# Performance work log

Measured on AMD Instinct MI355X. Metric: run time of the kernel, lower is better.

The kernel has to match this reference:

```python
import jax, jax.numpy as jnp
import numpy as np

B, S, D, H = 2, 2048, 1024, 16
HD = D // H  # head_dim = 64


def setup_inputs() -> dict:
    key = jax.random.key(0)
    ks = jax.random.split(key, 12)
    s = 1.0 / np.sqrt(D)
    return {
        "query": jax.random.normal(ks[0], (B, S, D), jnp.float32),
        "key": jax.random.normal(ks[1], (B, S, D), jnp.float32),
        "value": jax.random.normal(ks[2], (B, S, D), jnp.float32),
        "attention_mask": jnp.zeros((B, S, S), jnp.float32),
        "WQ_w": jax.random.normal(ks[3], (D, D), jnp.float32) * s,
        "WQ_b": jnp.zeros((D,), jnp.float32),
        "WK_w": jax.random.normal(ks[4], (D, D), jnp.float32) * s,
        "WK_b": jnp.zeros((D,), jnp.float32),
        "WV_w": jax.random.normal(ks[5], (D, D), jnp.float32) * s,
        "WV_b": jnp.zeros((D,), jnp.float32),
        "WO_w": jax.random.normal(ks[6], (D, D), jnp.float32) * s,
        "WO_b": jnp.zeros((D,), jnp.float32),
    }


def _split_heads(x):
    # [B,S,D] -> [B,H,S,HD]
    b, s, _ = x.shape
    return x.reshape(b, s, H, HD).transpose(0, 2, 1, 3)


def reference(query, key, value, attention_mask,
              WQ_w, WQ_b, WK_w, WK_b, WV_w, WV_b, WO_w, WO_b):
    Q = _split_heads(query @ WQ_w.T + WQ_b)   # [B,H,S,HD]
    K = _split_heads(key @ WK_w.T + WK_b)
    V = _split_heads(value @ WV_w.T + WV_b)
    scale = 1.0 / jnp.sqrt(jnp.float32(HD))
    scores = jnp.einsum('bhqd,bhkd->bhqk', Q, K) * scale
    scores = scores + attention_mask[:, None, :, :]
    attn = jax.nn.softmax(scores, axis=-1)    # dropout_prob=0.0 -> identity
    out = jnp.einsum('bhqk,bhkd->bhqd', attn, V)
    out = out.transpose(0, 2, 1, 3).reshape(query.shape[0], -1, D)
    return out @ WO_w.T + WO_b
```

## Files before the change

### kernel.cpp

```cpp
#include <hip/hip_runtime.h>
#include <math.h>


typedef _Float16 h8 __attribute__((ext_vector_type(8)));
typedef _Float16 h4 __attribute__((ext_vector_type(4)));
typedef float f4 __attribute__((ext_vector_type(4)));

#define MFMA16(a, b, c) __builtin_amdgcn_mfma_f32_16x16x32_f16((a), (b), (c), 0, 0, 0)
#define EXP2F(x) __builtin_amdgcn_exp2f(x)

static constexpr int Bn = 2, Sn = 2048, Dn = 1024, Hn = 16, HDn = 64;
static constexpr int Mn = Bn * Sn;
static constexpr int Kn = Dn;
static constexpr int Nn = Dn;
static constexpr int LDP = 72;
static constexpr float LOG2E = 1.4426950408889634f;

__device__ __forceinline__ void gload_lds16(const _Float16* g, _Float16* l) {
  __builtin_amdgcn_global_load_lds(
      (const __attribute__((address_space(1))) unsigned int*)g,
      (__attribute__((address_space(3))) unsigned int*)l, 16, 0, 0);
}

struct CvtJobs {
  const float* src[8];
  _Float16* dst[8];
  int n4[8];
  float scl[8];
};

__global__ __launch_bounds__(256) void cvt_kernel(CvtJobs j) {
  const int stride = gridDim.x * blockDim.x;
  const int t0 = blockIdx.x * blockDim.x + threadIdx.x;
#pragma unroll
  for (int k = 0; k < 8; ++k) {
    const float4* __restrict__ s = (const float4*)j.src[k];
    h4* __restrict__ d = (h4*)j.dst[k];
    const int n = j.n4[k];
    const float sc = j.scl[k];
    for (int i = t0; i < n; i += stride) {
      const float4 f = s[i];
      h4 h;
      h[0] = (_Float16)(f.x * sc); h[1] = (_Float16)(f.y * sc);
      h[2] = (_Float16)(f.z * sc); h[3] = (_Float16)(f.w * sc);
      d[i] = h;
    }
  }
}

struct QkvArgs {
  const _Float16* X[3];
  const _Float16* W[3];
  const float* bias[3];
  _Float16* out[3];
};

__global__ __launch_bounds__(256) void gemm_qkv(QkvArgs args) {
  const int z = blockIdx.z;
  const _Float16* __restrict__ X = args.X[z];
  const _Float16* __restrict__ W = args.W[z];
  const float* __restrict__ bias = args.bias[z];
  _Float16* __restrict__ out = args.out[z];

  __shared__ _Float16 As[128 * 64];
  __shared__ _Float16 Bs[128 * 64];

  const int t = threadIdx.x;
  const int lane = t & 63, wv = t >> 6;
  const int l15 = lane & 15, quad = lane >> 4;
  const int wm = (wv >> 1) * 64, wn = (wv & 1) * 64;
  const int n0 = blockIdx.x * 128, m0 = blockIdx.y * 128;

  f4 acc[4][4];
#pragma unroll
  for (int i = 0; i < 4; ++i)
#pragma unroll
    for (int j = 0; j < 4; ++j) {
      f4 zz = {0.f, 0.f, 0.f, 0.f};
      acc[i][j] = zz;
    }

  const int srow = lane >> 3, scol = (lane & 7) * 8;

  for (int k0 = 0; k0 < Kn; k0 += 64) {
    __syncthreads();
#pragma unroll
    for (int u = 0; u < 4; ++u) {
      const int s = wv * 4 + u;
      const int row = s * 8 + srow;
      gload_lds16(X + (size_t)(m0 + row) * Kn + k0 + scol, As + s * 512);
      gload_lds16(W + (size_t)(n0 + row) * Kn + k0 + scol, Bs + s * 512);
    }
    __syncthreads();
#pragma unroll
    for (int kk = 0; kk < 64; kk += 32) {
      h8 af[4], bfr[4];
#pragma unroll
      for (int i = 0; i < 4; ++i)
        af[i] = *(const h8*)&As[(wm + i * 16 + l15) * 64 + kk + quad * 8];
#pragma unroll
      for (int j = 0; j < 4; ++j)
        bfr[j] = *(const h8*)&Bs[(wn + j * 16 + l15) * 64 + kk + quad * 8];
#pragma unroll
      for (int i = 0; i < 4; ++i)
#pragma unroll
        for (int j = 0; j < 4; ++j)
          acc[i][j] = MFMA16(af[i], bfr[j], acc[i][j]);
    }
  }

  const float osc = (z == 0) ? (0.125f * LOG2E) : 1.0f;
  if (z != 2) {
#pragma unroll
    for (int j = 0; j < 4; ++j) {
      const int n = n0 + wn + j * 16 + l15;
      const float bvs = bias[n] * osc;
      const int hh = n >> 6, hd = n & 63;
#pragma unroll
      for (int i = 0; i < 4; ++i) {
        const int mb = m0 + wm + i * 16 + quad * 4;
        const int bb = mb >> 11;
#pragma unroll
        for (int r = 0; r < 4; ++r) {
          const int ss = (mb + r) & (Sn - 1);
          out[(((size_t)(bb * Hn + hh)) * Sn + ss) * HDn + hd] =
              (_Float16)(acc[i][j][r] * osc + bvs);
        }
      }
    }
  } else {
#pragma unroll
    for (int j = 0; j < 4; ++j) {
      const int n = n0 + wn + j * 16 + l15;
      const float bv = bias[n];
      const int hh = n >> 6, hd = n & 63;
#pragma unroll
      for (int i = 0; i < 4; ++i) {
        const int mb = m0 + wm + i * 16 + quad * 4;
        const int bb = mb >> 11, ss = mb & (Sn - 1);
        h4 hv;
#pragma unroll
        for (int r = 0; r < 4; ++r) hv[r] = (_Float16)(acc[i][j][r] + bv);
        *(h4*)(out + (((size_t)(bb * Hn + hh)) * HDn + hd) * Sn + ss) = hv;
      }
    }
  }
}

__global__ __launch_bounds__(256) void gemm_o(const _Float16* __restrict__ X,
                                              const _Float16* __restrict__ W,
                                              const float* __restrict__ bias,
                                              float* __restrict__ out) {
  __shared__ _Float16 As[128 * 64];
  __shared__ _Float16 Bs[128 * 64];

  const int t = threadIdx.x;
  const int lane = t & 63, wv = t >> 6;
  const int l15 = lane & 15, quad = lane >> 4;
  const int wm = (wv >> 1) * 64, wn = (wv & 1) * 64;
  const int n0 = blockIdx.x * 128, m0 = blockIdx.y * 128;

  f4 acc[4][4];
#pragma unroll
  for (int i = 0; i < 4; ++i)
#pragma unroll
    for (int j = 0; j < 4; ++j) {
      f4 zz = {0.f, 0.f, 0.f, 0.f};
      acc[i][j] = zz;
    }

  const int srow = lane >> 3, scol = (lane & 7) * 8;

  for (int k0 = 0; k0 < Kn; k0 += 64) {
    __syncthreads();
#pragma unroll
    for (int u = 0; u < 4; ++u) {
      const int s = wv * 4 + u;
      const int row = s * 8 + srow;
      gload_lds16(X + (size_t)(m0 + row) * Kn + k0 + scol, As + s * 512);
      gload_lds16(W + (size_t)(n0 + row) * Kn + k0 + scol, Bs + s * 512);
    }
    __syncthreads();
#pragma unroll
    for (int kk = 0; kk < 64; kk += 32) {
      h8 af[4], bfr[4];
#pragma unroll
      for (int i = 0; i < 4; ++i)
        af[i] = *(const h8*)&As[(wm + i * 16 + l15) * 64 + kk + quad * 8];
#pragma unroll
      for (int j = 0; j < 4; ++j)
        bfr[j] = *(const h8*)&Bs[(wn + j * 16 + l15) * 64 + kk + quad * 8];
#pragma unroll
      for (int i = 0; i < 4; ++i)
#pragma unroll
        for (int j = 0; j < 4; ++j)
          acc[i][j] = MFMA16(af[i], bfr[j], acc[i][j]);
    }
  }

#pragma unroll
  for (int j = 0; j < 4; ++j) {
    const int n = n0 + wn + j * 16 + l15;
    const float bv = bias[n];
#pragma unroll
    for (int i = 0; i < 4; ++i) {
      const int mb = m0 + wm + i * 16 + quad * 4;
#pragma unroll
      for (int r = 0; r < 4; ++r)
        out[(size_t)(mb + r) * Nn + n] = acc[i][j][r] + bv;
    }
  }
}

__global__ __launch_bounds__(512) void attn_kernel(
    const _Float16* __restrict__ Qh,
    const _Float16* __restrict__ Kh,
    const _Float16* __restrict__ Vt,
    const _Float16* __restrict__ maskh,
    _Float16* __restrict__ out) {
  __shared__ _Float16 smem[4 * 64 * LDP];

  const int t = threadIdx.x;
  const int w = t >> 6, lane = t & 63;
  const int l15 = lane & 15, quad = lane >> 4;
  const int g = w >> 2;
  const int wq = w & 3;

  const int bid = blockIdx.y * gridDim.x + blockIdx.x;
  const int xcd = bid & 7;
  const int idx = bid >> 3;
  const int bh = (xcd << 2) | (idx >> 5);
  const int qb = (idx & 31) * 64;

  const int b = bh >> 4, h = bh & 15;
  const size_t headoff = (size_t)bh * Sn * HDn;
  const _Float16* Qp = Qh + headoff;
  const _Float16* Kp = Kh + headoff;
  const _Float16* Vp = Vt + headoff;

  const int q0 = qb + wq * 16;
  const h8 qf0 = *(const h8*)(Qp + (size_t)(q0 + l15) * HDn + quad * 8);
  const h8 qf1 = *(const h8*)(Qp + (size_t)(q0 + l15) * HDn + 32 + quad * 8);

  const int kbase = g * (Sn / 2);
  const _Float16* mrow = maskh + ((size_t)b * Sn + q0 + l15) * Sn + kbase;

  float m_run = -INFINITY, l_part = 0.f;
  f4 o_acc[4];
#pragma unroll
  for (int nt = 0; nt < 4; ++nt) {
    f4 zz = {0.f, 0.f, 0.f, 0.f};
    o_acc[nt] = zz;
  }

  _Float16* Kg = smem + g * (64 * LDP);
  _Float16* Vg = smem + (2 + g) * (64 * LDP);

  const int tg = t & 255;
  const int srow = tg >> 3, sc8 = (tg & 7) * 8;
  const int srow1 = srow + 32;
  const int a = tg & 7;
  const int vb = ((a >> 2) & 1) * 32 + (a & 1) * 16 + ((a >> 1) & 1) * 4;

  constexpr int NT = (Sn / 2) / 64;

  uint4 kreg0, kreg1, vreg0, vreg1;
  uint2 mreg[4];
  auto kv_issue = [&](int kt) {
    kreg0 = *(const uint4*)(Kp + (size_t)(kbase + kt * 64 + srow) * HDn + sc8);
    vreg0 = *(const uint4*)(Vp + (size_t)srow * Sn + kbase + kt * 64 + sc8);
    kreg1 = *(const uint4*)(Kp + (size_t)(kbase + kt * 64 + srow1) * HDn + sc8);
    vreg1 = *(const uint4*)(Vp + (size_t)srow1 * Sn + kbase + kt * 64 + sc8);
  };
  auto m_issue = [&](int kt) {
#pragma unroll
    for (int ks = 0; ks < 4; ++ks)
      mreg[ks] = *(const uint2*)(mrow + kt * 64 + ks * 16 + quad * 4);
  };

  kv_issue(0);
  m_issue(0);

  for (int kt = 0; kt < NT; ++kt) {
    __syncthreads();
    *(uint4*)&Kg[srow * LDP + sc8] = kreg0;
    *(uint4*)&Kg[srow1 * LDP + sc8] = kreg1;
    *(uint2*)&Vg[srow * LDP + vb] = make_uint2(vreg0.x, vreg0.y);
    *(uint2*)&Vg[srow * LDP + vb + 8] = make_uint2(vreg0.z, vreg0.w);
    *(uint2*)&Vg[srow1 * LDP + vb] = make_uint2(vreg1.x, vreg1.y);
    *(uint2*)&Vg[srow1 * LDP + vb + 8] = make_uint2(vreg1.z, vreg1.w);
    __syncthreads();
    const int nx = (kt + 1 < NT) ? kt + 1 : kt;
    kv_issue(nx);

    f4 s[4];
#pragma unroll
    for (int ks = 0; ks < 4; ++ks) {
      const h4 mh = *(const h4*)&mreg[ks];
      f4 acc0;
#pragma unroll
      for (int r = 0; r < 4; ++r) acc0[r] = (float)mh[r];
      const h8 kf0 = *(const h8*)&Kg[(ks * 16 + l15) * LDP + quad * 8];
      const h8 kf1 = *(const h8*)&Kg[(ks * 16 + l15) * LDP + 32 + quad * 8];
      acc0 = MFMA16(kf0, qf0, acc0);
      s[ks] = MFMA16(kf1, qf1, acc0);
    }
    m_issue(nx);

    float mx = s[0][0];
#pragma unroll
    for (int ks = 0; ks < 4; ++ks)
#pragma unroll
      for (int r = 0; r < 4; ++r) mx = fmaxf(mx, s[ks][r]);
    mx = fmaxf(mx, __shfl_xor(mx, 16));
    mx = fmaxf(mx, __shfl_xor(mx, 32));
    if (!__all(mx - m_run <= 8.0f)) {
      const float nm = fmaxf(m_run, mx);
      const float alpha = EXP2F(m_run - nm);
      m_run = nm;
      l_part *= alpha;
#pragma unroll
      for (int nt = 0; nt < 4; ++nt)
#pragma unroll
        for (int r = 0; r < 4; ++r) o_acc[nt][r] *= alpha;
    }
    float sm = 0.f;
#pragma unroll
    for (int ks = 0; ks < 4; ++ks)
#pragma unroll
      for (int r = 0; r < 4; ++r) {
        s[ks][r] = EXP2F(s[ks][r] - m_run);
        sm += s[ks][r];
      }
    l_part += sm;

#pragma unroll
    for (int c = 0; c < 2; ++c) {
      h8 pf;
#pragma unroll
      for (int r = 0; r < 4; ++r) pf[r] = (_Float16)s[2 * c][r];
#pragma unroll
      for (int r = 0; r < 4; ++r) pf[4 + r] = (_Float16)s[2 * c + 1][r];
#pragma unroll
      for (int nt = 0; nt < 4; ++nt) {
        const h8 vf = *(const h8*)&Vg[(nt * 16 + l15) * LDP + c * 32 + quad * 8];
        o_acc[nt] = MFMA16(vf, pf, o_acc[nt]);
      }
    }
  }

  l_part += __shfl_xor(l_part, 16);
  l_part += __shfl_xor(l_part, 32);

  __syncthreads();
  float* Uex = (float*)smem;
  float* mex = Uex + 4 * 16 * LDP;
  float* lex = mex + 64;
  if (g == 1) {
#pragma unroll
    for (int nt = 0; nt < 4; ++nt)
      *(f4*)&Uex[wq * 16 * LDP + l15 * LDP + nt * 16 + quad * 4] = o_acc[nt];
    if (quad == 0) {
      mex[wq * 16 + l15] = m_run;
      lex[wq * 16 + l15] = l_part;
    }
  }
  __syncthreads();
  if (g == 0) {
    const float m1 = mex[wq * 16 + l15];
    const float l1 = lex[wq * 16 + l15];
    const float mm = fmaxf(m_run, m1);
    const float f0 = EXP2F(m_run - mm);
    const float f1 = EXP2F(m1 - mm);
    const float rl = 1.0f / (f0 * l_part + f1 * l1);
    _Float16* Ob = smem + 3 * (64 * LDP) + (w * 16) * LDP;
#pragma unroll
    for (int nt = 0; nt < 4; ++nt) {
      const f4 Ur = *(const f4*)&Uex[wq * 16 * LDP + l15 * LDP + nt * 16 + quad * 4];
      h4 ov;
#pragma unroll
      for (int r = 0; r < 4; ++r)
        ov[r] = (_Float16)((o_acc[nt][r] * f0 + Ur[r] * f1) * rl);
      *(h4*)&Ob[l15 * LDP + nt * 16 + quad * 4] = ov;
    }
    const int qr = lane >> 2;
    const int seg = (lane & 3) * 16;
    _Float16* dst = out + ((size_t)b * Sn + q0 + qr) * Dn + h * 64 + seg;
    *(uint4*)dst = *(const uint4*)&Ob[qr * LDP + seg];
    *(uint4*)(dst + 8) = *(const uint4*)&Ob[qr * LDP + seg + 8];
  }
}

extern "C" void kernel_launch(void* const* d_in, const int* in_sizes, int n_in,
                              void* d_out, int out_size, void* d_ws, size_t ws_size,
                              hipStream_t stream) {
  const float* q = (const float*)d_in[0];
  const float* k = (const float*)d_in[1];
  const float* v = (const float*)d_in[2];
  const float* mask = (const float*)d_in[3];
  const float* WQ = (const float*)d_in[4];
  const float* bQ = (const float*)d_in[5];
  const float* WK = (const float*)d_in[6];
  const float* bK = (const float*)d_in[7];
  const float* WV = (const float*)d_in[8];
  const float* bV = (const float*)d_in[9];
  const float* WO = (const float*)d_in[10];
  const float* bO = (const float*)d_in[11];

  _Float16* ws = (_Float16*)d_ws;
  const size_t MD = (size_t)Mn * Dn;
  const size_t DD = (size_t)Dn * Dn;
  const size_t SS = (size_t)Bn * Sn * Sn;
  _Float16* qh  = ws;
  _Float16* kh  = ws + MD;
  _Float16* vh  = ws + 2 * MD;
  _Float16* WQh = ws + 3 * MD;
  _Float16* WKh = WQh + DD;
  _Float16* WVh = WKh + DD;
  _Float16* WOh = WVh + DD;
  _Float16* Qh  = ws + 3 * MD + 4 * DD;
  _Float16* Kh  = Qh + MD;
  _Float16* Vt  = Kh + MD;
  _Float16* AO  = qh;
  const size_t used = 6 * MD + 4 * DD;
  _Float16* Mh = (ws_size >= (used + SS) * sizeof(_Float16))
                     ? (ws + used)
                     : (_Float16*)d_out;

  CvtJobs cj;
  cj.src[0] = q;    cj.dst[0] = qh;  cj.n4[0] = (int)(MD / 4);  cj.scl[0] = 1.f;
  cj.src[1] = k;    cj.dst[1] = kh;  cj.n4[1] = (int)(MD / 4);  cj.scl[1] = 1.f;
  cj.src[2] = v;    cj.dst[2] = vh;  cj.n4[2] = (int)(MD / 4);  cj.scl[2] = 1.f;
  cj.src[3] = WQ;   cj.dst[3] = WQh; cj.n4[3] = (int)(DD / 4);  cj.scl[3] = 1.f;
  cj.src[4] = WK;   cj.dst[4] = WKh; cj.n4[4] = (int)(DD / 4);  cj.scl[4] = 1.f;
  cj.src[5] = WV;   cj.dst[5] = WVh; cj.n4[5] = (int)(DD / 4);  cj.scl[5] = 1.f;
  cj.src[6] = WO;   cj.dst[6] = WOh; cj.n4[6] = (int)(DD / 4);  cj.scl[6] = 1.f;
  cj.src[7] = mask; cj.dst[7] = Mh;  cj.n4[7] = (int)(SS / 4);  cj.scl[7] = LOG2E;
  cvt_kernel<<<1024, 256, 0, stream>>>(cj);

  QkvArgs ga;
  ga.X[0] = qh; ga.W[0] = WQh; ga.bias[0] = bQ; ga.out[0] = Qh;
  ga.X[1] = kh; ga.W[1] = WKh; ga.bias[1] = bK; ga.out[1] = Kh;
  ga.X[2] = vh; ga.W[2] = WVh; ga.bias[2] = bV; ga.out[2] = Vt;
  gemm_qkv<<<dim3(Nn / 128, Mn / 128, 3), 256, 0, stream>>>(ga);

  attn_kernel<<<dim3(Sn / 64, Bn * Hn), 512, 0, stream>>>(Qh, Kh, Vt, Mh, AO);

  gemm_o<<<dim3(Nn / 128, Mn / 128), 256, 0, stream>>>(AO, WOh, bO, (float*)d_out);
}
```

Measured before the change: 305.0 us.

## Process two query sub-tiles per wave in attention to reuse K/V tiles

Each attention block now handles 128 query rows instead of 64, with every wave computing two 16-row query sub-tiles that share the same K and V fragments read from LDS. This halves global K/V traffic and LDS staging per query and raises MFMA work per load. It also drops the XCD-aware block remapping and adds a launch-bounds occupancy hint. The costs are higher register pressure, half as many blocks (512), and a two-pass epilogue with extra barriers.

```diff
diff --git a/kernel.cpp b/kernel.cpp
--- a/kernel.cpp
+++ b/kernel.cpp
@@ -212,7 +212,7 @@
   }
 }
 
-__global__ __launch_bounds__(512) void attn_kernel(
+__global__ __launch_bounds__(512, 4) void attn_kernel(
     const _Float16* __restrict__ Qh,
     const _Float16* __restrict__ Kh,
     const _Float16* __restrict__ Vt,
@@ -226,31 +226,32 @@
   const int g = w >> 2;
   const int wq = w & 3;
 
-  const int bid = blockIdx.y * gridDim.x + blockIdx.x;
-  const int xcd = bid & 7;
-  const int idx = bid >> 3;
-  const int bh = (xcd << 2) | (idx >> 5);
-  const int qb = (idx & 31) * 64;
-
+  const int bh = blockIdx.y;
   const int b = bh >> 4, h = bh & 15;
   const size_t headoff = (size_t)bh * Sn * HDn;
   const _Float16* Qp = Qh + headoff;
   const _Float16* Kp = Kh + headoff;
   const _Float16* Vp = Vt + headoff;
 
-  const int q0 = qb + wq * 16;
-  const h8 qf0 = *(const h8*)(Qp + (size_t)(q0 + l15) * HDn + quad * 8);
-  const h8 qf1 = *(const h8*)(Qp + (size_t)(q0 + l15) * HDn + 32 + quad * 8);
+  const int qb = blockIdx.x * 128;
+  const int q0 = qb + wq * 32;
+  const h8 qf00 = *(const h8*)(Qp + (size_t)(q0 + l15) * HDn + quad * 8);
+  const h8 qf01 = *(const h8*)(Qp + (size_t)(q0 + l15) * HDn + 32 + quad * 8);
+  const h8 qf10 = *(const h8*)(Qp + (size_t)(q0 + 16 + l15) * HDn + quad * 8);
+  const h8 qf11 = *(const h8*)(Qp + (size_t)(q0 + 16 + l15) * HDn + 32 + quad * 8);
 
   const int kbase = g * (Sn / 2);
-  const _Float16* mrow = maskh + ((size_t)b * Sn + q0 + l15) * Sn + kbase;
-
-  float m_run = -INFINITY, l_part = 0.f;
-  f4 o_acc[4];
+  const _Float16* mrow0 = maskh + ((size_t)b * Sn + q0 + l15) * Sn + kbase;
+  const _Float16* mrow1 = mrow0 + (size_t)16 * Sn;
+
+  float m_run0 = -INFINITY, l_part0 = 0.f;
+  float m_run1 = -INFINITY, l_part1 = 0.f;
+  f4 o0[4], o1[4];
 #pragma unroll
   for (int nt = 0; nt < 4; ++nt) {
     f4 zz = {0.f, 0.f, 0.f, 0.f};
-    o_acc[nt] = zz;
+    o0[nt] = zz;
+    o1[nt] = zz;
   }
 
   _Float16* Kg = smem + g * (64 * LDP);
@@ -265,7 +266,7 @@
   constexpr int NT = (Sn / 2) / 64;
 
   uint4 kreg0, kreg1, vreg0, vreg1;
-  uint2 mreg[4];
+  uint2 mreg0[4], mreg1[4];
   auto kv_issue = [&](int kt) {
     kreg0 = *(const uint4*)(Kp + (size_t)(kbase + kt * 64 + srow) * HDn + sc8);
     vreg0 = *(const uint4*)(Vp + (size_t)srow * Sn + kbase + kt * 64 + sc8);
@@ -274,8 +275,10 @@
   };
   auto m_issue = [&](int kt) {
 #pragma unroll
-    for (int ks = 0; ks < 4; ++ks)
-      mreg[ks] = *(const uint2*)(mrow + kt * 64 + ks * 16 + quad * 4);
+    for (int ks = 0; ks < 4; ++ks) {
+      mreg0[ks] = *(const uint2*)(mrow0 + kt * 64 + ks * 16 + quad * 4);
+      mreg1[ks] = *(const uint2*)(mrow1 + kt * 64 + ks * 16 + quad * 4);
+    }
   };
 
   kv_issue(0);
@@ -293,101 +296,154 @@
     const int nx = (kt + 1 < NT) ? kt + 1 : kt;
     kv_issue(nx);
 
-    f4 s[4];
+    f4 s0[4], s1[4];
 #pragma unroll
     for (int ks = 0; ks < 4; ++ks) {
-      const h4 mh = *(const h4*)&mreg[ks];
-      f4 acc0;
-#pragma unroll
-      for (int r = 0; r < 4; ++r) acc0[r] = (float)mh[r];
       const h8 kf0 = *(const h8*)&Kg[(ks * 16 + l15) * LDP + quad * 8];
       const h8 kf1 = *(const h8*)&Kg[(ks * 16 + l15) * LDP + 32 + quad * 8];
-      acc0 = MFMA16(kf0, qf0, acc0);
-      s[ks] = MFMA16(kf1, qf1, acc0);
+      const h4 mh0 = *(const h4*)&mreg0[ks];
+      const h4 mh1 = *(const h4*)&mreg1[ks];
+      f4 a0, a1;
+#pragma unroll
+      for (int r = 0; r < 4; ++r) { a0[r] = (float)mh0[r]; a1[r] = (float)mh1[r]; }
+      a0 = MFMA16(kf0, qf00, a0);
+      s0[ks] = MFMA16(kf1, qf01, a0);
+      a1 = MFMA16(kf0, qf10, a1);
+      s1[ks] = MFMA16(kf1, qf11, a1);
     }
     m_issue(nx);
 
-    float mx = s[0][0];
-#pragma unroll
-    for (int ks = 0; ks < 4; ++ks)
-#pragma unroll
-      for (int r = 0; r < 4; ++r) mx = fmaxf(mx, s[ks][r]);
-    mx = fmaxf(mx, __shfl_xor(mx, 16));
-    mx = fmaxf(mx, __shfl_xor(mx, 32));
-    if (!__all(mx - m_run <= 8.0f)) {
-      const float nm = fmaxf(m_run, mx);
-      const float alpha = EXP2F(m_run - nm);
-      m_run = nm;
-      l_part *= alpha;
-#pragma unroll
-      for (int nt = 0; nt < 4; ++nt)
-#pragma unroll
-        for (int r = 0; r < 4; ++r) o_acc[nt][r] *= alpha;
-    }
-    float sm = 0.f;
-#pragma unroll
-    for (int ks = 0; ks < 4; ++ks)
-#pragma unroll
-      for (int r = 0; r < 4; ++r) {
-        s[ks][r] = EXP2F(s[ks][r] - m_run);
-        sm += s[ks][r];
-      }
-    l_part += sm;
+    h8 pf0[2], pf1[2];
+    {
+      float mx = s0[0][0];
+#pragma unroll
+      for (int ks = 0; ks < 4; ++ks)
+#pragma unroll
+        for (int r = 0; r < 4; ++r) mx = fmaxf(mx, s0[ks][r]);
+      mx = fmaxf(mx, __shfl_xor(mx, 16));
+      mx = fmaxf(mx, __shfl_xor(mx, 32));
+      if (!__all(mx - m_run0 <= 8.0f)) {
+        const float nm = fmaxf(m_run0, mx);
+        const float al = EXP2F(m_run0 - nm);
+        m_run0 = nm;
+        l_part0 *= al;
+#pragma unroll
+        for (int nt = 0; nt < 4; ++nt)
+#pragma unroll
+          for (int r = 0; r < 4; ++r) o0[nt][r] *= al;
+      }
+      float sm = 0.f;
+#pragma unroll
+      for (int ks = 0; ks < 4; ++ks)
+#pragma unroll
+        for (int r = 0; r < 4; ++r) {
+          s0[ks][r] = EXP2F(s0[ks][r] - m_run0);
+          sm += s0[ks][r];
+        }
+      l_part0 += sm;
+#pragma unroll
+      for (int c = 0; c < 2; ++c)
+#pragma unroll
+        for (int r = 0; r < 4; ++r) {
+          pf0[c][r] = (_Float16)s0[2 * c][r];
+          pf0[c][4 + r] = (_Float16)s0[2 * c + 1][r];
+        }
+    }
+    {
+      float mx = s1[0][0];
+#pragma unroll
+      for (int ks = 0; ks < 4; ++ks)
+#pragma unroll
+        for (int r = 0; r < 4; ++r) mx = fmaxf(mx, s1[ks][r]);
+      mx = fmaxf(mx, __shfl_xor(mx, 16));
+      mx = fmaxf(mx, __shfl_xor(mx, 32));
+      if (!__all(mx - m_run1 <= 8.0f)) {
+        const float nm = fmaxf(m_run1, mx);
+        const float al = EXP2F(m_run1 - nm);
+        m_run1 = nm;
+        l_part1 *= al;
+#pragma unroll
+        for (int nt = 0; nt < 4; ++nt)
+#pragma unroll
+          for (int r = 0; r < 4; ++r) o1[nt][r] *= al;
+      }
+      float sm = 0.f;
+#pragma unroll
+      for (int ks = 0; ks < 4; ++ks)
+#pragma unroll
+        for (int r = 0; r < 4; ++r) {
+          s1[ks][r] = EXP2F(s1[ks][r] - m_run1);
+          sm += s1[ks][r];
+        }
+      l_part1 += sm;
+#pragma unroll
+      for (int c = 0; c < 2; ++c)
+#pragma unroll
+        for (int r = 0; r < 4; ++r) {
+          pf1[c][r] = (_Float16)s1[2 * c][r];
+          pf1[c][4 + r] = (_Float16)s1[2 * c + 1][r];
+        }
+    }
 
 #pragma unroll
     for (int c = 0; c < 2; ++c) {
-      h8 pf;
-#pragma unroll
-      for (int r = 0; r < 4; ++r) pf[r] = (_Float16)s[2 * c][r];
-#pragma unroll
-      for (int r = 0; r < 4; ++r) pf[4 + r] = (_Float16)s[2 * c + 1][r];
 #pragma unroll
       for (int nt = 0; nt < 4; ++nt) {
         const h8 vf = *(const h8*)&Vg[(nt * 16 + l15) * LDP + c * 32 + quad * 8];
-        o_acc[nt] = MFMA16(vf, pf, o_acc[nt]);
-      }
-    }
-  }
-
-  l_part += __shfl_xor(l_part, 16);
-  l_part += __shfl_xor(l_part, 32);
-
-  __syncthreads();
+        o0[nt] = MFMA16(vf, pf0[c], o0[nt]);
+        o1[nt] = MFMA16(vf, pf1[c], o1[nt]);
+      }
+    }
+  }
+
+  l_part0 += __shfl_xor(l_part0, 16);
+  l_part0 += __shfl_xor(l_part0, 32);
+  l_part1 += __shfl_xor(l_part1, 16);
+  l_part1 += __shfl_xor(l_part1, 32);
+
   float* Uex = (float*)smem;
   float* mex = Uex + 4 * 16 * LDP;
   float* lex = mex + 64;
-  if (g == 1) {
-#pragma unroll
-    for (int nt = 0; nt < 4; ++nt)
-      *(f4*)&Uex[wq * 16 * LDP + l15 * LDP + nt * 16 + quad * 4] = o_acc[nt];
-    if (quad == 0) {
-      mex[wq * 16 + l15] = m_run;
-      lex[wq * 16 + l15] = l_part;
-    }
-  }
-  __syncthreads();
-  if (g == 0) {
-    const float m1 = mex[wq * 16 + l15];
-    const float l1 = lex[wq * 16 + l15];
-    const float mm = fmaxf(m_run, m1);
-    const float f0 = EXP2F(m_run - mm);
-    const float f1 = EXP2F(m1 - mm);
-    const float rl = 1.0f / (f0 * l_part + f1 * l1);
-    _Float16* Ob = smem + 3 * (64 * LDP) + (w * 16) * LDP;
-#pragma unroll
-    for (int nt = 0; nt < 4; ++nt) {
-      const f4 Ur = *(const f4*)&Uex[wq * 16 * LDP + l15 * LDP + nt * 16 + quad * 4];
-      h4 ov;
-#pragma unroll
-      for (int r = 0; r < 4; ++r)
-        ov[r] = (_Float16)((o_acc[nt][r] * f0 + Ur[r] * f1) * rl);
-      *(h4*)&Ob[l15 * LDP + nt * 16 + quad * 4] = ov;
-    }
-    const int qr = lane >> 2;
-    const int seg = (lane & 3) * 16;
-    _Float16* dst = out + ((size_t)b * Sn + q0 + qr) * Dn + h * 64 + seg;
-    *(uint4*)dst = *(const uint4*)&Ob[qr * LDP + seg];
-    *(uint4*)(dst + 8) = *(const uint4*)&Ob[qr * LDP + seg + 8];
+#pragma unroll
+  for (int sub = 0; sub < 2; ++sub) {
+    const f4* oo = sub ? o1 : o0;
+    const float mr = sub ? m_run1 : m_run0;
+    const float lp = sub ? l_part1 : l_part0;
+    const int q0s = q0 + sub * 16;
+    __syncthreads();
+    if (g == 1) {
+#pragma unroll
+      for (int nt = 0; nt < 4; ++nt)
+        *(f4*)&Uex[wq * 16 * LDP + l15 * LDP + nt * 16 + quad * 4] = oo[nt];
+      if (quad == 0) {
+        mex[wq * 16 + l15] = mr;
+        lex[wq * 16 + l15] = lp;
+      }
+    }
+    __syncthreads();
+    if (g == 0) {
+      const float m1 = mex[wq * 16 + l15];
+      const float l1 = lex[wq * 16 + l15];
+      const float mm = fmaxf(mr, m1);
+      const float f0 = EXP2F(mr - mm);
+      const float f1 = EXP2F(m1 - mm);
+      const float rl = 1.0f / (f0 * lp + f1 * l1);
+      _Float16* Ob = smem + 3 * (64 * LDP) + (w * 16) * LDP;
+#pragma unroll
+      for (int nt = 0; nt < 4; ++nt) {
+        const f4 Ur = *(const f4*)&Uex[wq * 16 * LDP + l15 * LDP + nt * 16 + quad * 4];
+        h4 ov;
+#pragma unroll
+        for (int r = 0; r < 4; ++r)
+          ov[r] = (_Float16)((oo[nt][r] * f0 + Ur[r] * f1) * rl);
+        *(h4*)&Ob[l15 * LDP + nt * 16 + quad * 4] = ov;
+      }
+      const int qr = lane >> 2;
+      const int seg = (lane & 3) * 16;
+      _Float16* dst = out + ((size_t)b * Sn + q0s + qr) * Dn + h * 64 + seg;
+      *(uint4*)dst = *(const uint4*)&Ob[qr * LDP + seg];
+      *(uint4*)(dst + 8) = *(const uint4*)&Ob[qr * LDP + seg + 8];
+    }
   }
 }
 
@@ -444,7 +500,7 @@
   ga.X[2] = vh; ga.W[2] = WVh; ga.bias[2] = bV; ga.out[2] = Vt;
   gemm_qkv<<<dim3(Nn / 128, Mn / 128, 3), 256, 0, stream>>>(ga);
 
-  attn_kernel<<<dim3(Sn / 64, Bn * Hn), 512, 0, stream>>>(Qh, Kh, Vt, Mh, AO);
+  attn_kernel<<<dim3(Sn / 128, Bn * Hn), 512, 0, stream>>>(Qh, Kh, Vt, Mh, AO);
 
   gemm_o<<<dim3(Nn / 128, Mn / 128), 256, 0, stream>>>(AO, WOh, bO, (float*)d_out);
 }
```

Result: slower. 330.9 us (+8.5%).
